# Kernel optimization log

Measured on AMD Instinct MI355X. Metric: run time of the kernel, lower is better.

The kernel has to match this reference:

```python
import jax, jax.numpy as jnp
import numpy as np

N = 100000      # nodes
E = 3200000     # edges (avg degree 32)
IN = 128        # in_channels
H = 32          # hidden dim
OUT = 64        # out_channels
L = 31          # number of SGConv layers


def setup_inputs() -> dict:
    key = jax.random.key(0)
    ks = jax.random.split(key, 10)
    x = jax.random.normal(ks[0], (N, IN), dtype=jnp.float32)
    edge_index = jax.random.randint(ks[1], (2, E), 0, N, dtype=jnp.int32)
    s = 0.05
    W1 = jax.random.normal(ks[2], (H, IN), dtype=jnp.float32) * s
    b1 = jnp.zeros((H,), dtype=jnp.float32)
    Wc = jax.random.normal(ks[3], (L, H, H), dtype=jnp.float32) * s
    bc = jnp.zeros((L, H), dtype=jnp.float32)
    W32 = jax.random.normal(ks[4], (OUT, 32 * H), dtype=jnp.float32) * s
    b32 = jnp.zeros((OUT,), dtype=jnp.float32)
    return {"x": x, "edge_index": edge_index, "W1": W1, "b1": b1,
            "Wc": Wc, "bc": bc, "W32": W32, "b32": b32}


def mynorm(t):
    # min/max over feature axis (dim=1 of [N, C]; last axis in general)
    mn = jnp.min(t, axis=-1, keepdims=True)
    mx = jnp.max(t, axis=-1, keepdims=True)
    return 2.0 * (t - mn) / (mx - mn + 1e-8) - 1.0


def reference(x, edge_index, W1, b1, Wc, bc, W32, b32):
    n = x.shape[0]
    loops = jnp.arange(n, dtype=edge_index.dtype)
    row = jnp.concatenate([edge_index[0], loops])  # source
    col = jnp.concatenate([edge_index[1], loops])  # target
    # symmetric GCN normalization (PyG gcn_norm, add_self_loops=True)
    deg = jax.ops.segment_sum(jnp.ones_like(row, dtype=x.dtype), col, num_segments=n)
    dis = jnp.where(deg > 0, jax.lax.rsqrt(deg), 0.0)
    nrm = (dis[row] * dis[col])[:, None]  # [E+N, 1]

    def prop(h):
        # out[col] += norm * h[row]
        return jax.ops.segment_sum(h[row] * nrm, col, num_segments=n)

    x0 = mynorm(jax.nn.relu(x @ W1.T + b1))  # [N, 32]

    def step(h, p):
        W, b = p
        y = prop(h) @ W.T + b  # SGConv K=1: propagate then linear
        return y, y

    _, ys = jax.lax.scan(step, x0, (Wc, bc))  # [31, N, 32]
    xs = jnp.concatenate([x0[None], ys], axis=0)  # [32, N, 32]
    m = mynorm(xs)
    # xx1 = x1; xxk = mynorm(xk) - mynorm(x_{k-2}); original uses raw x16 at slot 16
    feats = [x0, xs[1]]
    for k in range(2, 32):
        feats.append(xs[k] if k == 16 else m[k] - m[k - 2])
    cat = jnp.concatenate(feats, axis=1)  # [N, 1024]
    return cat @ W32.T + b32  # [N, 64]
```

## Files before the change

### kernel.cpp

```cpp
#include <hip/hip_runtime.h>
#include <hip/hip_fp16.h>

#define NN 100000
#define NE 3200000

__global__ __launch_bounds__(256) void k_deg(const int* __restrict__ col, int* __restrict__ deg) {
    int e = blockIdx.x * 256 + threadIdx.x;
    if (e < NE) atomicAdd(&deg[col[e]], 1);
}

__global__ __launch_bounds__(256) void k_bsum(const int* __restrict__ deg, int* __restrict__ bsum) {
    __shared__ int s[256];
    int t = threadIdx.x, i = blockIdx.x * 256 + t;
    s[t] = (i < NN) ? deg[i] : 0;
    __syncthreads();
    for (int st = 128; st > 0; st >>= 1) {
        if (t < st) s[t] += s[t + st];
        __syncthreads();
    }
    if (t == 0) bsum[blockIdx.x] = s[0];
}

__global__ __launch_bounds__(512) void k_scanb(int* __restrict__ bsum, int nb) {
    __shared__ int s[512];
    int t = threadIdx.x;
    s[t] = (t < nb) ? bsum[t] : 0;
    __syncthreads();
    for (int off = 1; off < 512; off <<= 1) {
        int v = (t >= off) ? s[t - off] : 0;
        __syncthreads();
        s[t] += v;
        __syncthreads();
    }
    if (t < nb) bsum[t] = (t == 0) ? 0 : s[t - 1];
}

__global__ __launch_bounds__(256) void k_colptr(const int* __restrict__ deg, const int* __restrict__ bsum,
                                                int* __restrict__ colptr) {
    __shared__ int s[256];
    int t = threadIdx.x, i = blockIdx.x * 256 + t;
    int v = (i < NN) ? deg[i] : 0;
    s[t] = v;
    __syncthreads();
    for (int off = 1; off < 256; off <<= 1) {
        int u = (t >= off) ? s[t - off] : 0;
        __syncthreads();
        s[t] += u;
        __syncthreads();
    }
    if (i <= NN) colptr[i] = bsum[blockIdx.x] + s[t] - v;
}

__global__ __launch_bounds__(256) void k_dis(int* __restrict__ degdis) {
    int i = blockIdx.x * 256 + threadIdx.x;
    if (i < NN) {
        int d = degdis[i];
        ((float*)degdis)[i] = 1.0f / sqrtf((float)(d + 1));
    }
}

__global__ __launch_bounds__(256) void k_scatter(const int* __restrict__ ei, const int* __restrict__ colptr,
                                                 int* __restrict__ cursor, int* __restrict__ csr_row) {
    int e = blockIdx.x * 256 + threadIdx.x;
    if (e < NE) {
        int c = ei[NE + e], r = ei[e];
        int pos = colptr[c] + atomicAdd(&cursor[c], 1);
        csr_row[pos] = r;
    }
}

__global__ __launch_bounds__(256) void k_x0(const float* __restrict__ x, const float* __restrict__ W1,
                                            const float* __restrict__ b1, const float* __restrict__ W32,
                                            const float* __restrict__ b32, const float* __restrict__ dis,
                                            __half* __restrict__ h0, __half* __restrict__ ring0,
                                            float* __restrict__ out, float* __restrict__ Mhat,
                                            float* __restrict__ SCar) {
    __shared__ float sW1[32 * 128];
    __shared__ float sW32[64 * 32];
    __shared__ float sb1[32], sb32[64];
    int t = threadIdx.x;
    if (blockIdx.x == 0 && t == 0) SCar[0] = 1.0f;
    for (int i = t; i < 4096; i += 256) sW1[i] = W1[i];
    for (int i = t; i < 2048; i += 256) sW32[i] = W32[(i >> 5) * 1024 + (i & 31)];
    if (t < 32) sb1[t] = b1[t];
    if (t < 64) sb32[t] = b32[t];
    __syncthreads();
    int node = blockIdx.x * 256 + t;
    if (node >= NN) return;

    float acc[32];
#pragma unroll
    for (int c = 0; c < 32; c++) acc[c] = sb1[c];
    const float4* xr4 = (const float4*)(x + (long)node * 128);
    for (int q = 0; q < 32; q++) {
        float4 xv = xr4[q];
#pragma unroll
        for (int c = 0; c < 32; c++) {
            acc[c] += xv.x * sW1[c * 128 + q * 4] + xv.y * sW1[c * 128 + q * 4 + 1] +
                      xv.z * sW1[c * 128 + q * 4 + 2] + xv.w * sW1[c * 128 + q * 4 + 3];
        }
    }
    float mn = 1e30f, mx = -1e30f;
#pragma unroll
    for (int c = 0; c < 32; c++) {
        acc[c] = fmaxf(acc[c], 0.f);
        mn = fminf(mn, acc[c]);
        mx = fmaxf(mx, acc[c]);
    }
    float inv = 2.f / (mx - mn + 1e-8f);
#pragma unroll
    for (int c = 0; c < 32; c++) acc[c] = inv * (acc[c] - mn) - 1.f;
    float sc = dis[node];
    __half2* hr = (__half2*)(h0 + (long)node * 32);
#pragma unroll
    for (int q = 0; q < 16; q++) hr[q] = __floats2half2_rn(sc * acc[2 * q], sc * acc[2 * q + 1]);
    if (t == 0 && (blockIdx.x & 15) == 0) atomicMax((int*)&Mhat[0], __float_as_int(sc));
    float mn2 = 1e30f, mx2 = -1e30f;
#pragma unroll
    for (int c = 0; c < 32; c++) {
        mn2 = fminf(mn2, acc[c]);
        mx2 = fmaxf(mx2, acc[c]);
    }
    float inv2 = 2.f / (mx2 - mn2 + 1e-8f);
    __half2* rr = (__half2*)(ring0 + (long)node * 32);
#pragma unroll
    for (int q = 0; q < 16; q++)
        rr[q] = __floats2half2_rn(inv2 * (acc[2 * q] - mn2) - 1.f, inv2 * (acc[2 * q + 1] - mn2) - 1.f);
    float* orow = out + (long)node * 64;
    for (int o = 0; o < 64; o++) {
        float a = sb32[o];
#pragma unroll
        for (int j = 0; j < 32; j++) a += sW32[o * 32 + j] * acc[j];
        orow[o] = a;
    }
}

__global__ __launch_bounds__(256, 3) void k_layer(const __half* __restrict__ hin, __half* __restrict__ hout,
                                                  __half* __restrict__ ring, const float* __restrict__ dis,
                                                  const int* __restrict__ colptr, const int* __restrict__ csr_row,
                                                  const float* __restrict__ Wck, const float* __restrict__ bck,
                                                  const float* __restrict__ W32k, float* __restrict__ out,
                                                  float* __restrict__ Mhat, float* __restrict__ SCar, int k,
                                                  int rawfeat) {
    __shared__ float sWc[32 * 33];
    __shared__ float sW[64 * 33];
    __shared__ float sbc[32];
    int t = threadIdx.x;
    float SCin = SCar[k - 1];
    float SCk = SCin * fmaxf(Mhat[k - 1], 1e-30f);
    if (t == 0) SCar[k] = SCk;
    float invSCk = 1.0f / SCk;
    for (int i = t; i < 1024; i += 256) sWc[(i >> 5) * 33 + (i & 31)] = Wck[i];
    for (int i = t; i < 2048; i += 256) sW[(i >> 5) * 33 + (i & 31)] = W32k[(i >> 5) * 1024 + (i & 31)];
    if (t < 32) sbc[t] = bck[t];
    __syncthreads();

    int wave = t >> 6, lane = t & 63;
    int sub = lane >> 3, q = lane & 7;
    int node = blockIdx.x * 32 + wave * 8 + sub;
    int sl = sub * 8;

    const uint2* __restrict__ h2 = (const uint2*)hin;
    int e0 = colptr[node], e1 = colptr[node + 1];
    float di = dis[node];

    float a0, a1, a2, a3, b0 = 0.f, b1 = 0.f, b2 = 0.f, b3 = 0.f;
    {
        uint2 u = h2[(long)node * 8 + q];
        float2 lo = __half22float2(*(__half2*)&u.x);
        float2 hi = __half22float2(*(__half2*)&u.y);
        a0 = lo.x; a1 = lo.y; a2 = hi.x; a3 = hi.y;
    }
    int base = e0;
    while (base + 8 <= e1) {
        int r = csr_row[base + q];
#pragma unroll
        for (int j = 0; j < 8; j += 2) {
            int r0 = __shfl(r, sl + j, 64);
            int r1 = __shfl(r, sl + j + 1, 64);
            uint2 u0 = h2[(long)r0 * 8 + q];
            uint2 u1 = h2[(long)r1 * 8 + q];
            float2 lo0 = __half22float2(*(__half2*)&u0.x), hi0 = __half22float2(*(__half2*)&u0.y);
            float2 lo1 = __half22float2(*(__half2*)&u1.x), hi1 = __half22float2(*(__half2*)&u1.y);
            a0 += lo0.x; a1 += lo0.y; a2 += hi0.x; a3 += hi0.y;
            b0 += lo1.x; b1 += lo1.y; b2 += hi1.x; b3 += hi1.y;
        }
        base += 8;
    }
    int rem = e1 - base;
    if (rem > 0) {
        int r = (q < rem) ? csr_row[base + q] : 0;
        for (int j = 0; j < rem; j++) {
            int rj = __shfl(r, sl + j, 64);
            uint2 u = h2[(long)rj * 8 + q];
            float2 lo = __half22float2(*(__half2*)&u.x), hi = __half22float2(*(__half2*)&u.y);
            a0 += lo.x; a1 += lo.y; a2 += hi.x; a3 += hi.y;
        }
    }
    float g0 = di * (a0 + b0), g1 = di * (a1 + b1), g2 = di * (a2 + b2), g3 = di * (a3 + b3);

    const float* wr0 = &sWc[(4 * q + 0) * 33];
    const float* wr1 = &sWc[(4 * q + 1) * 33];
    const float* wr2 = &sWc[(4 * q + 2) * 33];
    const float* wr3 = &sWc[(4 * q + 3) * 33];
    float y0 = 0.f, y1 = 0.f, y2 = 0.f, y3 = 0.f;
#pragma unroll
    for (int s = 0; s < 8; s++) {
        float t0 = __shfl(g0, sl + s, 64);
        float t1 = __shfl(g1, sl + s, 64);
        float t2 = __shfl(g2, sl + s, 64);
        float t3 = __shfl(g3, sl + s, 64);
        int jb = 4 * s;
        y0 += wr0[jb] * t0 + wr0[jb + 1] * t1 + wr0[jb + 2] * t2 + wr0[jb + 3] * t3;
        y1 += wr1[jb] * t0 + wr1[jb + 1] * t1 + wr1[jb + 2] * t2 + wr1[jb + 3] * t3;
        y2 += wr2[jb] * t0 + wr2[jb + 1] * t1 + wr2[jb + 2] * t2 + wr2[jb + 3] * t3;
        y3 += wr3[jb] * t0 + wr3[jb + 1] * t1 + wr3[jb + 2] * t2 + wr3[jb + 3] * t3;
    }
    y0 = SCin * y0 + sbc[4 * q + 0];
    y1 = SCin * y1 + sbc[4 * q + 1];
    y2 = SCin * y2 + sbc[4 * q + 2];
    y3 = SCin * y3 + sbc[4 * q + 3];

    {
        __half2 p0 = __floats2half2_rn(di * y0 * invSCk, di * y1 * invSCk);
        __half2 p1 = __floats2half2_rn(di * y2 * invSCk, di * y3 * invSCk);
        uint2 pw;
        pw.x = *(unsigned int*)&p0;
        pw.y = *(unsigned int*)&p1;
        ((uint2*)hout)[(long)node * 8 + q] = pw;
    }

    float mn = fminf(fminf(y0, y1), fminf(y2, y3));
    float mx = fmaxf(fmaxf(y0, y1), fmaxf(y2, y3));
#pragma unroll
    for (int m = 1; m < 8; m <<= 1) {
        mn = fminf(mn, __shfl_xor(mn, m, 64));
        mx = fmaxf(mx, __shfl_xor(mx, m, 64));
    }
    float inv = 2.f / (mx - mn + 1e-8f);
    float mv0 = inv * (y0 - mn) - 1.f, mv1 = inv * (y1 - mn) - 1.f;
    float mv2 = inv * (y2 - mn) - 1.f, mv3 = inv * (y3 - mn) - 1.f;

    if ((blockIdx.x & 15) == 0 && q == 0) {
        float rowmax = fmaxf(fabsf(mn), fabsf(mx));
        atomicMax((int*)&Mhat[k], __float_as_int(di * rowmax * invSCk));
    }

    float f0, f1, f2, f3;
    if (rawfeat) {
        f0 = y0; f1 = y1; f2 = y2; f3 = y3;
    } else {
        uint2 rv = ((const uint2*)ring)[(long)node * 8 + q];
        float2 rlo = __half22float2(*(__half2*)&rv.x);
        float2 rhi = __half22float2(*(__half2*)&rv.y);
        f0 = mv0 - rlo.x; f1 = mv1 - rlo.y; f2 = mv2 - rhi.x; f3 = mv3 - rhi.y;
    }
    {
        __half2 p0 = __floats2half2_rn(mv0, mv1);
        __half2 p1 = __floats2half2_rn(mv2, mv3);
        uint2 pw;
        pw.x = *(unsigned int*)&p0;
        pw.y = *(unsigned int*)&p1;
        ((uint2*)ring)[(long)node * 8 + q] = pw;
    }

    float o0 = 0.f, o1 = 0.f, o2 = 0.f, o3 = 0.f, o4 = 0.f, o5 = 0.f, o6 = 0.f, o7 = 0.f;
#pragma unroll
    for (int s = 0; s < 8; s++) {
        float t0 = __shfl(f0, sl + s, 64);
        float t1 = __shfl(f1, sl + s, 64);
        float t2 = __shfl(f2, sl + s, 64);
        float t3 = __shfl(f3, sl + s, 64);
        int jb = 4 * s;
        const float* w = &sW[(8 * q) * 33 + jb];
        o0 += w[0] * t0 + w[1] * t1 + w[2] * t2 + w[3] * t3; w += 33;
        o1 += w[0] * t0 + w[1] * t1 + w[2] * t2 + w[3] * t3; w += 33;
        o2 += w[0] * t0 + w[1] * t1 + w[2] * t2 + w[3] * t3; w += 33;
        o3 += w[0] * t0 + w[1] * t1 + w[2] * t2 + w[3] * t3; w += 33;
        o4 += w[0] * t0 + w[1] * t1 + w[2] * t2 + w[3] * t3; w += 33;
        o5 += w[0] * t0 + w[1] * t1 + w[2] * t2 + w[3] * t3; w += 33;
        o6 += w[0] * t0 + w[1] * t1 + w[2] * t2 + w[3] * t3; w += 33;
        o7 += w[0] * t0 + w[1] * t1 + w[2] * t2 + w[3] * t3;
    }
    float4* op = (float4*)(out + (long)node * 64 + 8 * q);
    float4 v0 = op[0], v1 = op[1];
    v0.x += o0; v0.y += o1; v0.z += o2; v0.w += o3;
    v1.x += o4; v1.y += o5; v1.z += o6; v1.w += o7;
    op[0] = v0;
    op[1] = v1;
}

extern "C" void kernel_launch(void* const* d_in, const int* in_sizes, int n_in, void* d_out, int out_size,
                              void* d_ws, size_t ws_size, hipStream_t stream) {
    const float* x = (const float*)d_in[0];
    const int* ei = (const int*)d_in[1];
    const float* W1 = (const float*)d_in[2];
    const float* b1 = (const float*)d_in[3];
    const float* Wc = (const float*)d_in[4];
    const float* bc = (const float*)d_in[5];
    const float* W32 = (const float*)d_in[6];
    const float* b32 = (const float*)d_in[7];
    float* out = (float*)d_out;

    int* deg = (int*)d_ws;
    int* cursor = deg + NN;
    float* Mhat = (float*)(cursor + NN);
    float* SCar = Mhat + 64;
    int* colptr = (int*)(SCar + 64);
    int* bsum = colptr + 100004;
    int* csr_row = bsum + 1024;
    __half* h0 = (__half*)(csr_row + NE);
    __half* h1 = h0 + (long)NN * 32;
    __half* ring = h1 + (long)NN * 32;
    float* dis = (float*)deg;

    hipMemsetAsync(deg, 0, (2 * NN + 128) * sizeof(int), stream);
    k_deg<<<(NE + 255) / 256, 256, 0, stream>>>(ei + NE, deg);
    int NB = (NN + 255) / 256;
    k_bsum<<<NB, 256, 0, stream>>>(deg, bsum);
    k_scanb<<<1, 512, 0, stream>>>(bsum, NB);
    k_colptr<<<NB, 256, 0, stream>>>(deg, bsum, colptr);
    k_dis<<<(NN + 255) / 256, 256, 0, stream>>>(deg);
    k_scatter<<<(NE + 255) / 256, 256, 0, stream>>>(ei, colptr, cursor, csr_row);
    k_x0<<<NB, 256, 0, stream>>>(x, W1, b1, W32, b32, dis, h0, ring, out, Mhat, SCar);

    for (int k = 1; k <= 31; k++) {
        const __half* hin = (k & 1) ? h0 : h1;
        __half* hout = (k & 1) ? h1 : h0;
        __half* ringk = ring + (long)(k & 1) * NN * 32;
        int raw = (k == 1 || k == 16) ? 1 : 0;
        k_layer<<<3125, 256, 0, stream>>>(hin, hout, ringk, dis, colptr, csr_row, Wc + (k - 1) * 1024,
                                          bc + (k - 1) * 32, W32 + 32 * k, out, Mhat, SCar, k, raw);
    }
}
```

Baseline: 2.741 ms.

## Stage neighbor indices in LDS and spread each node's gather across the wave

The layer kernel now preloads up to 64 CSR neighbor indices per node into shared memory. Each node's edge gather is then split across all 8 sub-groups of the wave and combined with an xor-shuffle reduction, instead of one 8-lane group walking its own node's edges serially. This evens out load imbalance between nodes of different degree and adds parallel memory requests per node. The cost is extra LDS use, a barrier, and shuffle reductions per node. Separately, the CSR scatter is split into 8 passes by destination range to improve write locality, at the price of reading the edge list 8 times.

```diff
diff --git a/kernel.cpp b/kernel.cpp
--- a/kernel.cpp
+++ b/kernel.cpp
@@ -3,6 +3,7 @@
 
 #define NN 100000
 #define NE 3200000
+#define NB8 12500
 
 __global__ __launch_bounds__(256) void k_deg(const int* __restrict__ col, int* __restrict__ deg) {
     int e = blockIdx.x * 256 + threadIdx.x;
@@ -60,12 +61,16 @@
 }
 
 __global__ __launch_bounds__(256) void k_scatter(const int* __restrict__ ei, const int* __restrict__ colptr,
-                                                 int* __restrict__ cursor, int* __restrict__ csr_row) {
+                                                 int* __restrict__ cursor, int* __restrict__ csr_row, int p) {
     int e = blockIdx.x * 256 + threadIdx.x;
     if (e < NE) {
-        int c = ei[NE + e], r = ei[e];
-        int pos = colptr[c] + atomicAdd(&cursor[c], 1);
-        csr_row[pos] = r;
+        int c = ei[NE + e];
+        int lo = p * NB8;
+        if (c >= lo && c < lo + NB8) {
+            int r = ei[e];
+            int pos = colptr[c] + atomicAdd(&cursor[c], 1);
+            csr_row[pos] = r;
+        }
     }
 }
 
@@ -145,6 +150,7 @@
     __shared__ float sWc[32 * 33];
     __shared__ float sW[64 * 33];
     __shared__ float sbc[32];
+    __shared__ int sIdx[32][65];
     int t = threadIdx.x;
     float SCin = SCar[k - 1];
     float SCk = SCin * fmaxf(Mhat[k - 1], 1e-30f);
@@ -153,56 +159,85 @@
     for (int i = t; i < 1024; i += 256) sWc[(i >> 5) * 33 + (i & 31)] = Wck[i];
     for (int i = t; i < 2048; i += 256) sW[(i >> 5) * 33 + (i & 31)] = W32k[(i >> 5) * 1024 + (i & 31)];
     if (t < 32) sbc[t] = bck[t];
-    __syncthreads();
 
     int wave = t >> 6, lane = t & 63;
     int sub = lane >> 3, q = lane & 7;
-    int node = blockIdx.x * 32 + wave * 8 + sub;
-    int sl = sub * 8;
+    int nodebase = blockIdx.x * 32 + wave * 8;
+    int mynode = nodebase + sub;
+
+    int e0s = colptr[nodebase + (lane & 7)];
+    int e1s = colptr[nodebase + (lane & 7) + 1];
+
+#pragma unroll
+    for (int n = 0; n < 8; n++) {
+        int e0n = __shfl(e0s, n, 64);
+        int dn = __shfl(e1s, n, 64) - e0n;
+        if (dn > 64) dn = 64;
+        int wn = wave * 8 + n;
+        for (int i = lane; i < dn; i += 64) sIdx[wn][i] = csr_row[e0n + i];
+    }
+    __syncthreads();
 
     const uint2* __restrict__ h2 = (const uint2*)hin;
-    int e0 = colptr[node], e1 = colptr[node + 1];
-    float di = dis[node];
-
-    float a0, a1, a2, a3, b0 = 0.f, b1 = 0.f, b2 = 0.f, b3 = 0.f;
+    float di = dis[mynode];
+
+    float g0, g1, g2, g3;
     {
-        uint2 u = h2[(long)node * 8 + q];
+        uint2 u = h2[(long)mynode * 8 + q];
         float2 lo = __half22float2(*(__half2*)&u.x);
         float2 hi = __half22float2(*(__half2*)&u.y);
-        a0 = lo.x; a1 = lo.y; a2 = hi.x; a3 = hi.y;
-    }
-    int base = e0;
-    while (base + 8 <= e1) {
-        int r = csr_row[base + q];
-#pragma unroll
-        for (int j = 0; j < 8; j += 2) {
-            int r0 = __shfl(r, sl + j, 64);
-            int r1 = __shfl(r, sl + j + 1, 64);
-            uint2 u0 = h2[(long)r0 * 8 + q];
-            uint2 u1 = h2[(long)r1 * 8 + q];
+        g0 = lo.x; g1 = lo.y; g2 = hi.x; g3 = hi.y;
+    }
+
+#pragma unroll 1
+    for (int n = 0; n < 8; n++) {
+        int e0 = __shfl(e0s, n, 64);
+        int deg = __shfl(e1s, n, 64) - e0;
+        int degl = (deg > 64) ? 64 : deg;
+        int wn = wave * 8 + n;
+        float a0 = 0.f, a1 = 0.f, a2 = 0.f, a3 = 0.f;
+        int j = sub;
+        while (j + 8 < degl) {
+            int i0 = sIdx[wn][j];
+            int i1 = sIdx[wn][j + 8];
+            uint2 u0 = h2[(long)i0 * 8 + q];
+            uint2 u1 = h2[(long)i1 * 8 + q];
             float2 lo0 = __half22float2(*(__half2*)&u0.x), hi0 = __half22float2(*(__half2*)&u0.y);
             float2 lo1 = __half22float2(*(__half2*)&u1.x), hi1 = __half22float2(*(__half2*)&u1.y);
-            a0 += lo0.x; a1 += lo0.y; a2 += hi0.x; a3 += hi0.y;
-            b0 += lo1.x; b1 += lo1.y; b2 += hi1.x; b3 += hi1.y;
-        }
-        base += 8;
-    }
-    int rem = e1 - base;
-    if (rem > 0) {
-        int r = (q < rem) ? csr_row[base + q] : 0;
-        for (int j = 0; j < rem; j++) {
-            int rj = __shfl(r, sl + j, 64);
-            uint2 u = h2[(long)rj * 8 + q];
+            a0 += lo0.x + lo1.x; a1 += lo0.y + lo1.y;
+            a2 += hi0.x + hi1.x; a3 += hi0.y + hi1.y;
+            j += 16;
+        }
+        if (j < degl) {
+            int i0 = sIdx[wn][j];
+            uint2 u = h2[(long)i0 * 8 + q];
             float2 lo = __half22float2(*(__half2*)&u.x), hi = __half22float2(*(__half2*)&u.y);
             a0 += lo.x; a1 += lo.y; a2 += hi.x; a3 += hi.y;
         }
-    }
-    float g0 = di * (a0 + b0), g1 = di * (a1 + b1), g2 = di * (a2 + b2), g3 = di * (a3 + b3);
+        if (deg > 64) {
+            for (int jj = 64 + sub; jj < deg; jj += 8) {
+                int idx = csr_row[e0 + jj];
+                uint2 u = h2[(long)idx * 8 + q];
+                float2 lo = __half22float2(*(__half2*)&u.x), hi = __half22float2(*(__half2*)&u.y);
+                a0 += lo.x; a1 += lo.y; a2 += hi.x; a3 += hi.y;
+            }
+        }
+#pragma unroll
+        for (int m = 8; m < 64; m <<= 1) {
+            a0 += __shfl_xor(a0, m, 64);
+            a1 += __shfl_xor(a1, m, 64);
+            a2 += __shfl_xor(a2, m, 64);
+            a3 += __shfl_xor(a3, m, 64);
+        }
+        if (sub == n) { g0 += a0; g1 += a1; g2 += a2; g3 += a3; }
+    }
+    g0 *= di; g1 *= di; g2 *= di; g3 *= di;
 
     const float* wr0 = &sWc[(4 * q + 0) * 33];
     const float* wr1 = &sWc[(4 * q + 1) * 33];
     const float* wr2 = &sWc[(4 * q + 2) * 33];
     const float* wr3 = &sWc[(4 * q + 3) * 33];
+    int sl = sub * 8;
     float y0 = 0.f, y1 = 0.f, y2 = 0.f, y3 = 0.f;
 #pragma unroll
     for (int s = 0; s < 8; s++) {
@@ -227,7 +262,7 @@
         uint2 pw;
         pw.x = *(unsigned int*)&p0;
         pw.y = *(unsigned int*)&p1;
-        ((uint2*)hout)[(long)node * 8 + q] = pw;
+        ((uint2*)hout)[(long)mynode * 8 + q] = pw;
     }
 
     float mn = fminf(fminf(y0, y1), fminf(y2, y3));
@@ -250,7 +285,7 @@
     if (rawfeat) {
         f0 = y0; f1 = y1; f2 = y2; f3 = y3;
     } else {
-        uint2 rv = ((const uint2*)ring)[(long)node * 8 + q];
+        uint2 rv = ((const uint2*)ring)[(long)mynode * 8 + q];
         float2 rlo = __half22float2(*(__half2*)&rv.x);
         float2 rhi = __half22float2(*(__half2*)&rv.y);
         f0 = mv0 - rlo.x; f1 = mv1 - rlo.y; f2 = mv2 - rhi.x; f3 = mv3 - rhi.y;
@@ -261,7 +296,7 @@
         uint2 pw;
         pw.x = *(unsigned int*)&p0;
         pw.y = *(unsigned int*)&p1;
-        ((uint2*)ring)[(long)node * 8 + q] = pw;
+        ((uint2*)ring)[(long)mynode * 8 + q] = pw;
     }
 
     float o0 = 0.f, o1 = 0.f, o2 = 0.f, o3 = 0.f, o4 = 0.f, o5 = 0.f, o6 = 0.f, o7 = 0.f;
@@ -282,7 +317,7 @@
         o6 += w[0] * t0 + w[1] * t1 + w[2] * t2 + w[3] * t3; w += 33;
         o7 += w[0] * t0 + w[1] * t1 + w[2] * t2 + w[3] * t3;
     }
-    float4* op = (float4*)(out + (long)node * 64 + 8 * q);
+    float4* op = (float4*)(out + (long)mynode * 64 + 8 * q);
     float4 v0 = op[0], v1 = op[1];
     v0.x += o0; v0.y += o1; v0.z += o2; v0.w += o3;
     v1.x += o4; v1.y += o5; v1.z += o6; v1.w += o7;
@@ -321,7 +356,8 @@
     k_scanb<<<1, 512, 0, stream>>>(bsum, NB);
     k_colptr<<<NB, 256, 0, stream>>>(deg, bsum, colptr);
     k_dis<<<(NN + 255) / 256, 256, 0, stream>>>(deg);
-    k_scatter<<<(NE + 255) / 256, 256, 0, stream>>>(ei, colptr, cursor, csr_row);
+    for (int p = 0; p < 8; p++)
+        k_scatter<<<(NE + 255) / 256, 256, 0, stream>>>(ei, colptr, cursor, csr_row, p);
     k_x0<<<NB, 256, 0, stream>>>(x, W1, b1, W32, b32, dis, h0, ring, out, Mhat, SCar);
 
     for (int k = 1; k <= 31; k++) {
```

Result: slower. 2.969 ms (+8.3%).
